# Performance work log

Measured on AMD Instinct MI355X. Metric: run time of the kernel, lower is better.

Reference implementation:

```python
import jax, jax.numpy as jnp
import numpy as np

NEG_INF = -1e9


def setup_inputs() -> dict:
    key = jax.random.key(0)
    k1, k2, k3 = jax.random.split(key, 3)
    B, C, Q, D = 32, 2048, 128, 128
    context = jax.random.normal(k1, (B, C, D), dtype=jnp.float32)
    query = jax.random.normal(k2, (B, Q, D), dtype=jnp.float32)
    # Dense(1, use_bias=False) over concat([c, q, c*q]) -> weight vector of length 3*D
    w = jax.random.normal(k3, (3 * D,), dtype=jnp.float32) * (1.0 / np.sqrt(3 * D))
    query_mask = jnp.ones((B, Q), dtype=jnp.int32)
    return {"context": context, "query": query, "w": w, "query_mask": query_mask}


def reference(context, query, w, query_mask):
    # context: [B, C, D], query: [B, Q, D], w: [3D], query_mask: [B, Q]
    D = context.shape[-1]
    w1, w2, w3 = w[:D], w[D:2 * D], w[2 * D:]
    # Trilinear similarity, exactly equal to Dense(1)(concat([c_tiled, q_tiled, c*q]))
    # S[b,c,q] = context[b,c]·w1 + query[b,q]·w2 + (context[b,c]*w3)·query[b,q]
    S = (context @ w1)[:, :, None] \
        + (query @ w2)[:, None, :] \
        + jnp.einsum('bcd,bqd->bcq', context * w3, query)  # [B, C, Q]
    mask_add = (1.0 - query_mask.astype(jnp.float32))[:, None, :] * NEG_INF
    S = S + mask_add
    a = jax.nn.softmax(S, axis=2)                  # context-to-query attention [B, C, Q]
    c2q = jnp.einsum('bcq,bqd->bcd', a, query)     # [B, C, D]
    b = jax.nn.softmax(jnp.max(S, axis=2), axis=1) # query-to-context weights [B, C]
    q2c = jnp.einsum('bc,bcd->bd', b, context)[:, None, :]  # [B, 1, D]
    q2c = jnp.broadcast_to(q2c, context.shape)     # tile over c_len
    out = jnp.concatenate([context, c2q, context * c2q, context * q2c], axis=-1)
    return out  # [B, C, 4D]
```

## Files before the change

### kernel.cpp

```cpp
#include <hip/hip_runtime.h>
#include <cstdint>

#define B_ 32
#define C_ 2048
#define Q_ 128
#define D_ 128
#define CT 64
#define OFF_ 8.0f
#define NEG_INF_F (-1.0e9f)

typedef __attribute__((ext_vector_type(8))) short bf16x8;
typedef __attribute__((ext_vector_type(4))) float f32x4;

__device__ inline short bf16_rne(float v) {
    unsigned u = __float_as_uint(v);
    return (short)((u + 0x7FFFu + ((u >> 16) & 1u)) >> 16);
}
__device__ inline void split_f32(float v, short& h, short& l) {
    unsigned u  = __float_as_uint(v);
    unsigned hb = u & 0xffff0000u;
    float lo = v - __uint_as_float(hb);
    h = (short)(hb >> 16);
    l = (short)(__float_as_uint(lo) >> 16);
}

__global__ __launch_bounds__(256)
void cqa_prep(const float* __restrict__ qry, const float* __restrict__ w,
              const int* __restrict__ qmask, float* __restrict__ qw2e_g,
              unsigned short* __restrict__ qw3Hi, unsigned short* __restrict__ qTHi)
{
    const int b = blockIdx.y, ch = blockIdx.x;
    const int t = threadIdx.x;
    const float* qb = qry + (size_t)b * Q_ * D_;

    if (t < 32) {
        int rl = t >> 1, part = t & 1;
        int q = ch * 16 + rl;
        const float* p  = qb + q * D_ + part * 64;
        const float* wp = w + D_ + part * 64;
        float s = 0.f;
        #pragma unroll
        for (int j = 0; j < 64; j += 4) {
            float4 a4 = *(const float4*)(p + j);
            float4 w4 = *(const float4*)(wp + j);
            s += a4.x*w4.x + a4.y*w4.y + a4.z*w4.z + a4.w*w4.w;
        }
        s += __shfl_xor(s, 1, 2);
        if (!part) {
            float madd = (1.0f - (float)qmask[b * Q_ + q]) * NEG_INF_F;
            qw2e_g[b * Q_ + q] = s + madd;
        }
    }
    #pragma unroll
    for (int i = 0; i < 8; ++i) {
        int idx = t + i * 256;
        int ql = idx >> 7, d = idx & 127;
        int q = ch * 16 + ql;
        float v = qb[q * D_ + d];
        qw3Hi[((size_t)b * Q_ + q) * D_ + d] = (unsigned short)bf16_rne(v * w[2 * D_ + d]);
        qTHi[((size_t)b * D_ + d) * Q_ + q]  = (unsigned short)bf16_rne(v);
    }
}

__device__ __forceinline__ void stage_b(const unsigned short* __restrict__ gH,
                                        int col0, short* sb, int wv, int lane)
{
    #pragma unroll
    for (int j = 0; j < 2; ++j) {
        int seg = wv * 2 + j;
        int li  = seg * 64 + lane;
        int row = li >> 2;
        int col = (li & 3) * 8;
        __builtin_amdgcn_global_load_lds(
            (const __attribute__((address_space(1))) void*)(gH + (size_t)row * 128 + col0 + col),
            (__attribute__((address_space(3))) void*)(sb + seg * 512), 16, 0, 0);
    }
}

__global__ __launch_bounds__(256, 5)
void cqa_main(const float* __restrict__ ctx, const float* __restrict__ w,
              const float* __restrict__ qw2e_g,
              const unsigned short* __restrict__ qw3Hi, const unsigned short* __restrict__ qTHi,
              float* __restrict__ out, float* __restrict__ part, float* __restrict__ denp_g)
{
    __shared__ __align__(16) char smem[27008];
    short* SB   = (short*)smem;
    short* PHi  = (short*)(smem + 8192);
    float* Tr   = (float*)smem;
    float* red  = (float*)smem;
    float* mlds = (float*)(smem + 25600);
    float* slds = (float*)(smem + 25856);
    float* cw1  = (float*)(smem + 26112);
    float* qw2e = (float*)(smem + 26368);
    float* dred = (float*)(smem + 26880);

    const int b   = blockIdx.y;
    const int c0  = blockIdx.x * CT;
    const int tid = threadIdx.x;
    const int lane = tid & 63;
    const int wv   = tid >> 6;
    const int w16  = wv * 16;
    const int lm   = lane & 15;
    const int lg   = lane >> 4;
    const int lk   = lg * 8;

    const float* ctxb = ctx + ((size_t)b * C_ + c0) * D_;
    const unsigned short* qw3Hb = qw3Hi + (size_t)b * Q_ * D_;
    const unsigned short* qTHb  = qTHi + (size_t)b * Q_ * D_;

    stage_b(qw3Hb, 0, SB, wv, lane);

    if (tid < Q_) qw2e[tid] = qw2e_g[b * Q_ + tid];

    const float* arow = ctxb + (size_t)(w16 + lm) * D_;
    bf16x8 aHr[4], aLr[4];
    float cws = 0.f;
    #pragma unroll
    for (int t = 0; t < 4; ++t) {
        float4 v0 = *(const float4*)(arow + t * 32 + lk);
        float4 v1 = *(const float4*)(arow + t * 32 + lk + 4);
        float4 w0 = *(const float4*)(w + t * 32 + lk);
        float4 w1v = *(const float4*)(w + t * 32 + lk + 4);
        cws += v0.x*w0.x + v0.y*w0.y + v0.z*w0.z + v0.w*w0.w
             + v1.x*w1v.x + v1.y*w1v.y + v1.z*w1v.z + v1.w*w1v.w;
        float vv[8] = {v0.x, v0.y, v0.z, v0.w, v1.x, v1.y, v1.z, v1.w};
        #pragma unroll
        for (int i = 0; i < 8; ++i) {
            short hh, ll; split_f32(vv[i], hh, ll);
            aHr[t][i] = hh; aLr[t][i] = ll;
        }
    }
    cws += __shfl_xor(cws, 16, 64);
    cws += __shfl_xor(cws, 32, 64);
    if (lane < 16) cw1[w16 + lm] = cws;
    __syncthreads();

    float qe[8];
    #pragma unroll
    for (int f = 0; f < 8; ++f) qe[f] = qw2e[f * 16 + lm];
    float cwr[4];
    #pragma unroll
    for (int r = 0; r < 4; ++r) cwr[r] = cw1[w16 + lg * 4 + r];

    const f32x4 vzero = {0.f, 0.f, 0.f, 0.f};
    f32x4 acc[8];
    #pragma unroll
    for (int f = 0; f < 8; ++f) acc[f] = vzero;

    #pragma unroll
    for (int t = 0; t < 4; ++t) {
        if (t < 3) stage_b(qw3Hb, (t + 1) * 32, ((t + 1) & 1) ? PHi : SB, wv, lane);
        const short* sb = (t & 1) ? PHi : SB;
        bf16x8 aH = aHr[t], aL = aLr[t];
        #pragma unroll
        for (int f = 0; f < 8; ++f) {
            bf16x8 bH = *(const bf16x8*)(sb + (f * 16 + lm) * 32 + lk);
            acc[f] = __builtin_amdgcn_mfma_f32_16x16x32_bf16(aH, bH, acc[f], 0, 0, 0);
            acc[f] = __builtin_amdgcn_mfma_f32_16x16x32_bf16(aL, bH, acc[f], 0, 0, 0);
        }
        __syncthreads();
    }

    bf16x8 qa[2][4];
    #pragma unroll
    for (int ds = 0; ds < 2; ++ds)
        #pragma unroll
        for (int t = 0; t < 4; ++t)
            qa[ds][t] = *(const bf16x8*)(qTHb + (size_t)(ds * 64 + w16 + lm) * 128 + t * 32 + lk);

    #pragma unroll
    for (int r = 0; r < 4; ++r) {
        float sv[8];
        float mx = -3.0e38f;
        #pragma unroll
        for (int f = 0; f < 8; ++f) {
            sv[f] = acc[f][r] + qe[f];
            mx = fmaxf(mx, sv[f]);
        }
        mx = fmaxf(mx, __shfl_xor(mx, 1, 16));
        mx = fmaxf(mx, __shfl_xor(mx, 2, 16));
        mx = fmaxf(mx, __shfl_xor(mx, 4, 16));
        mx = fmaxf(mx, __shfl_xor(mx, 8, 16));
        int lrow = w16 + lg * 4 + r;
        float s = 0.f;
        #pragma unroll
        for (int f = 0; f < 8; ++f) {
            float p = __expf(sv[f] - mx);
            s += p;
            PHi[lrow * 136 + f * 16 + lm] = bf16_rne(p);
        }
        s += __shfl_xor(s, 1, 16);
        s += __shfl_xor(s, 2, 16);
        s += __shfl_xor(s, 4, 16);
        s += __shfl_xor(s, 8, 16);
        if (lm == 0) { mlds[lrow] = mx + cwr[r]; slds[lrow] = 1.0f / s; }
    }
    __syncthreads();

    f32x4 acc2[2][4];
    #pragma unroll
    for (int ds = 0; ds < 2; ++ds)
        #pragma unroll
        for (int fc = 0; fc < 4; ++fc) acc2[ds][fc] = vzero;

    #pragma unroll
    for (int t = 0; t < 4; ++t) {
        #pragma unroll
        for (int fc = 0; fc < 4; ++fc) {
            bf16x8 bP = *(const bf16x8*)(PHi + (fc * 16 + lm) * 136 + t * 32 + lk);
            acc2[0][fc] = __builtin_amdgcn_mfma_f32_16x16x32_bf16(qa[0][t], bP, acc2[0][fc], 0, 0, 0);
            acc2[1][fc] = __builtin_amdgcn_mfma_f32_16x16x32_bf16(qa[1][t], bP, acc2[1][fc], 0, 0, 0);
        }
    }
    __syncthreads();

    const int rsel = tid >> 5;
    const int dd   = (tid & 31) * 4;
    float4 qacc = {0.f, 0.f, 0.f, 0.f};
    float denp = 0.f;
    #pragma unroll
    for (int p = 0; p < 2; ++p) {
        #pragma unroll
        for (int fq = 0; fq < 2; ++fq) {
            int fc = 2 * p + fq;
            float ic = slds[fc * 16 + lm];
            int cl = fq * 16 + lm;
            #pragma unroll
            for (int ds = 0; ds < 2; ++ds) {
                f32x4 v = acc2[ds][fc];
                float4 o;
                o.x = v[0] * ic; o.y = v[1] * ic; o.z = v[2] * ic; o.w = v[3] * ic;
                *(float4*)(Tr + cl * 132 + ds * 64 + w16 + lg * 4) = o;
            }
        }
        __syncthreads();
        #pragma unroll
        for (int i = 0; i < 4; ++i) {
            int cl  = i * 8 + rsel;
            int row = p * 32 + cl;
            float4 a  = *(const float4*)(Tr + cl * 132 + dd);
            float4 cv = *(const float4*)(ctxb + (size_t)row * D_ + dd);
            float wgt = __expf(mlds[row] - OFF_);
            size_t obase = ((size_t)b * C_ + c0 + row) * (4 * D_);
            float4 pr;
            pr.x = cv.x*a.x; pr.y = cv.y*a.y; pr.z = cv.z*a.z; pr.w = cv.w*a.w;
            *(float4*)(out + obase + dd)          = cv;
            *(float4*)(out + obase + D_ + dd)     = a;
            *(float4*)(out + obase + 2 * D_ + dd) = pr;
            qacc.x += wgt * cv.x; qacc.y += wgt * cv.y;
            qacc.z += wgt * cv.z; qacc.w += wgt * cv.w;
            denp += wgt;
        }
        __syncthreads();
    }

    *(float4*)(red + rsel * 128 + dd) = qacc;
    if ((tid & 31) == 0) dred[rsel] = denp;
    __syncthreads();
    if (tid < 128) {
        float s = 0.f;
        #pragma unroll
        for (int rr = 0; rr < 8; ++rr) s += red[rr * 128 + tid];
        part[((size_t)b * 32 + blockIdx.x) * 128 + tid] = s;
    }
    if (tid == 0) {
        float s = 0.f;
        #pragma unroll
        for (int rr = 0; rr < 8; ++rr) s += dred[rr];
        denp_g[b * 32 + blockIdx.x] = s;
    }
}

__global__ __launch_bounds__(128)
void cqa_q2c(const float* __restrict__ part, const float* __restrict__ denp_g,
             float* __restrict__ q2c)
{
    int b = blockIdx.x, d = threadIdx.x;
    float den = 0.f;
    #pragma unroll
    for (int j = 0; j < 32; ++j) den += denp_g[b * 32 + j];
    float s = 0.f;
    #pragma unroll
    for (int j = 0; j < 32; ++j) s += part[((size_t)b * 32 + j) * 128 + d];
    q2c[b * 128 + d] = s / den;
}

__global__ __launch_bounds__(256)
void cqa_out4(const float* __restrict__ ctx, const float* __restrict__ q2c,
              float* __restrict__ out)
{
    size_t i = (size_t)blockIdx.x * 256 + threadIdx.x;
    const size_t n4 = (size_t)B_*C_*D_/4;
    if (i >= n4) return;
    size_t bc = i >> 5;
    int d4 = (int)(i & 31);
    int b  = (int)(bc >> 11);
    float4 c4 = reinterpret_cast<const float4*>(ctx)[i];
    float4 g4 = reinterpret_cast<const float4*>(q2c)[b*32 + d4];
    float4 o;
    o.x = c4.x*g4.x; o.y = c4.y*g4.y; o.z = c4.z*g4.z; o.w = c4.w*g4.w;
    reinterpret_cast<float4*>(out)[bc*128 + 96 + d4] = o;
}

extern "C" void kernel_launch(void* const* d_in, const int* in_sizes, int n_in,
                              void* d_out, int out_size, void* d_ws, size_t ws_size,
                              hipStream_t stream)
{
    const float* ctx   = (const float*)d_in[0];
    const float* qry   = (const float*)d_in[1];
    const float* w     = (const float*)d_in[2];
    const int*   qmask = (const int*)d_in[3];
    float* out = (float*)d_out;
    float* ws  = (float*)d_ws;

    float* part    = ws;
    float* denp_g  = ws + 131072;
    float* q2c     = ws + 132096;
    float* qw2e_g  = ws + 136192;
    unsigned short* bf = (unsigned short*)(ws + 140288);
    unsigned short* qw3Hi = bf;
    unsigned short* qTHi  = bf + 524288;

    cqa_prep<<<dim3(8, B_), 256, 0, stream>>>(qry, w, qmask, qw2e_g, qw3Hi, qTHi);
    cqa_main<<<dim3(C_/CT, B_), 256, 0, stream>>>(ctx, w, qw2e_g, qw3Hi, qTHi,
                                                  out, part, denp_g);
    cqa_q2c<<<B_, 128, 0, stream>>>(part, denp_g, q2c);
    cqa_out4<<<(int)(((size_t)B_*C_*D_/4 + 255)/256), 256, 0, stream>>>(ctx, q2c, out);
}
```

Baseline: 54.15 us.

## Stage all query tiles up front and fuse q2c reduction into output kernel

```diff
diff --git a/kernel.cpp b/kernel.cpp
--- a/kernel.cpp
+++ b/kernel.cpp
@@ -77,22 +77,22 @@
     }
 }
 
-__global__ __launch_bounds__(256, 5)
+__global__ __launch_bounds__(256, 4)
 void cqa_main(const float* __restrict__ ctx, const float* __restrict__ w,
               const float* __restrict__ qw2e_g,
               const unsigned short* __restrict__ qw3Hi, const unsigned short* __restrict__ qTHi,
               float* __restrict__ out, float* __restrict__ part, float* __restrict__ denp_g)
 {
-    __shared__ __align__(16) char smem[27008];
+    __shared__ __align__(16) char smem[34176];
     short* SB   = (short*)smem;
-    short* PHi  = (short*)(smem + 8192);
+    short* PHi  = (short*)smem;
     float* Tr   = (float*)smem;
     float* red  = (float*)smem;
-    float* mlds = (float*)(smem + 25600);
-    float* slds = (float*)(smem + 25856);
-    float* cw1  = (float*)(smem + 26112);
-    float* qw2e = (float*)(smem + 26368);
-    float* dred = (float*)(smem + 26880);
+    float* mlds = (float*)(smem + 32768);
+    float* slds = (float*)(smem + 33024);
+    float* cw1  = (float*)(smem + 33280);
+    float* qw2e = (float*)(smem + 33536);
+    float* dred = (float*)(smem + 34048);
 
     const int b   = blockIdx.y;
     const int c0  = blockIdx.x * CT;
@@ -108,7 +108,9 @@
     const unsigned short* qw3Hb = qw3Hi + (size_t)b * Q_ * D_;
     const unsigned short* qTHb  = qTHi + (size_t)b * Q_ * D_;
 
-    stage_b(qw3Hb, 0, SB, wv, lane);
+    #pragma unroll
+    for (int t = 0; t < 4; ++t)
+        stage_b(qw3Hb, t * 32, SB + t * 4096, wv, lane);
 
     if (tid < Q_) qw2e[tid] = qw2e_g[b * Q_ + tid];
 
@@ -149,8 +151,7 @@
 
     #pragma unroll
     for (int t = 0; t < 4; ++t) {
-        if (t < 3) stage_b(qw3Hb, (t + 1) * 32, ((t + 1) & 1) ? PHi : SB, wv, lane);
-        const short* sb = (t & 1) ? PHi : SB;
+        const short* sb = SB + t * 4096;
         bf16x8 aH = aHr[t], aL = aLr[t];
         #pragma unroll
         for (int f = 0; f < 8; ++f) {
@@ -158,8 +159,8 @@
             acc[f] = __builtin_amdgcn_mfma_f32_16x16x32_bf16(aH, bH, acc[f], 0, 0, 0);
             acc[f] = __builtin_amdgcn_mfma_f32_16x16x32_bf16(aL, bH, acc[f], 0, 0, 0);
         }
-        __syncthreads();
-    }
+    }
+    __syncthreads();
 
     bf16x8 qa[2][4];
     #pragma unroll
@@ -271,35 +272,37 @@
     }
 }
 
-__global__ __launch_bounds__(128)
-void cqa_q2c(const float* __restrict__ part, const float* __restrict__ denp_g,
-             float* __restrict__ q2c)
-{
-    int b = blockIdx.x, d = threadIdx.x;
+__global__ __launch_bounds__(256)
+void cqa_out4(const float* __restrict__ ctx, const float* __restrict__ part,
+              const float* __restrict__ denp_g, float* __restrict__ out)
+{
+    const int b = blockIdx.y, ch = blockIdx.x;
+    const int tid = threadIdx.x;
+    __shared__ float q2s[128];
+
     float den = 0.f;
-    #pragma unroll
+    #pragma unroll 8
     for (int j = 0; j < 32; ++j) den += denp_g[b * 32 + j];
-    float s = 0.f;
-    #pragma unroll
-    for (int j = 0; j < 32; ++j) s += part[((size_t)b * 32 + j) * 128 + d];
-    q2c[b * 128 + d] = s / den;
-}
-
-__global__ __launch_bounds__(256)
-void cqa_out4(const float* __restrict__ ctx, const float* __restrict__ q2c,
-              float* __restrict__ out)
-{
-    size_t i = (size_t)blockIdx.x * 256 + threadIdx.x;
-    const size_t n4 = (size_t)B_*C_*D_/4;
-    if (i >= n4) return;
-    size_t bc = i >> 5;
-    int d4 = (int)(i & 31);
-    int b  = (int)(bc >> 11);
-    float4 c4 = reinterpret_cast<const float4*>(ctx)[i];
-    float4 g4 = reinterpret_cast<const float4*>(q2c)[b*32 + d4];
-    float4 o;
-    o.x = c4.x*g4.x; o.y = c4.y*g4.y; o.z = c4.z*g4.z; o.w = c4.w*g4.w;
-    reinterpret_cast<float4*>(out)[bc*128 + 96 + d4] = o;
+    if (tid < 128) {
+        float s = 0.f;
+        #pragma unroll 8
+        for (int j = 0; j < 32; ++j) s += part[((size_t)b * 32 + j) * 128 + tid];
+        q2s[tid] = s / den;
+    }
+    __syncthreads();
+
+    const float* cb = ctx + ((size_t)b * C_ + ch * 64) * D_;
+    float* ob = out + ((size_t)b * C_ + ch * 64) * (4 * D_);
+    #pragma unroll
+    for (int k = 0; k < 8; ++k) {
+        int i  = tid + k * 256;
+        int rl = i >> 5, d4 = (i & 31) * 4;
+        float4 c4 = *(const float4*)(cb + (size_t)rl * D_ + d4);
+        float4 g4 = *(const float4*)(q2s + d4);
+        float4 o;
+        o.x = c4.x*g4.x; o.y = c4.y*g4.y; o.z = c4.z*g4.z; o.w = c4.w*g4.w;
+        *(float4*)(ob + (size_t)rl * (4 * D_) + 3 * D_ + d4) = o;
+    }
 }
 
 extern "C" void kernel_launch(void* const* d_in, const int* in_sizes, int n_in,
@@ -315,15 +318,13 @@
 
     float* part    = ws;
     float* denp_g  = ws + 131072;
-    float* q2c     = ws + 132096;
-    float* qw2e_g  = ws + 136192;
-    unsigned short* bf = (unsigned short*)(ws + 140288);
+    float* qw2e_g  = ws + 132096;
+    unsigned short* bf = (unsigned short*)(ws + 136192);
     unsigned short* qw3Hi = bf;
     unsigned short* qTHi  = bf + 524288;
 
     cqa_prep<<<dim3(8, B_), 256, 0, stream>>>(qry, w, qmask, qw2e_g, qw3Hi, qTHi);
     cqa_main<<<dim3(C_/CT, B_), 256, 0, stream>>>(ctx, w, qw2e_g, qw3Hi, qTHi,
                                                   out, part, denp_g);
-    cqa_q2c<<<B_, 128, 0, stream>>>(part, denp_g, q2c);
-    cqa_out4<<<(int)(((size_t)B_*C_*D_/4 + 255)/256), 256, 0, stream>>>(ctx, q2c, out);
-}
+    cqa_out4<<<dim3(C_/64, B_), 256, 0, stream>>>(ctx, part, denp_g, out);
+}
```

Measured after the change: 52.75 us. 2.6% less time.
